# Performance work log

Hardware: AMD Instinct MI355X
Metric: run time of the kernel (lower is better)

## Reference

```python
import jax, jax.numpy as jnp
import numpy as np

# tf.image.rgb_to_grayscale luma weights; grayscale->rgb duplicates channels, so the
# rgb->gray after an identical per-channel gather reduces to scaling by sum(weights).
RGB_WSUM = np.float32(0.2989 + 0.5870 + 0.1140)


def _inverse_logpolar_indices(H, W):
    """Nearest-neighbor gather indices mapping a log-polar image (theta rows,
    rho cols) back to Cartesian coordinates (inverse log-polar remap)."""
    cy, cx = (H - 1) / 2.0, (W - 1) / 2.0
    ys, xs = np.meshgrid(np.arange(H, dtype=np.float64),
                         np.arange(W, dtype=np.float64), indexing='ij')
    dy, dx = ys - cy, xs - cx
    r = np.sqrt(dx * dx + dy * dy)
    rmax = np.sqrt(cx * cx + cy * cy)
    rho = np.where(r > 0.5, np.log(np.maximum(r, 1e-6)) / np.log(rmax) * (W - 1), 0.0)
    theta = (np.arctan2(dy, dx) + np.pi) / (2.0 * np.pi) * (H - 1)
    rho_i = np.clip(np.rint(rho), 0, W - 1).astype(np.int32)
    th_i = np.clip(np.rint(theta), 0, H - 1).astype(np.int32)
    return jnp.asarray(th_i), jnp.asarray(rho_i)  # each (H, W)


def setup_inputs() -> dict:
    key = jax.random.key(0)
    B, H, W, C = 1, 256, 256, 512
    inputs = jax.random.normal(key, (B, H, W, C), dtype=jnp.float32)
    return {"inputs": inputs}


def reference(inputs) -> jnp.ndarray:
    B, H, W, C = inputs.shape  # H == W required by the original layer's transpose/reshape
    # tf.transpose(tf.squeeze(inputs,0)) reverses all dims: (H,W,C) -> (C,W,H);
    # each channel is then tf.reshape'd to (H,W) (identity in memory for H==W).
    x = jnp.transpose(inputs[0], (2, 1, 0))  # (C, W, H) == (C, H, W) layout for square
    th_i, rho_i = _inverse_logpolar_indices(H, W)
    # Vectorized over channels: identical gather for every channel (replaces tf.map_fn).
    warped = x[:, th_i, rho_i]  # (C, H, W) irregular gather
    out = warped * RGB_WSUM      # gray->rgb (tile) -> warp -> rgb->gray collapses to a scale
    # tf.reshape((C,H,W) -> self.shape=(1,H,W,C)) is a raw row-major reshape (faithful).
    return jnp.reshape(out, (1, H, W, C))
```

## Files before the change

### kernel.cpp

```cpp
#include <hip/hip_runtime.h>
#include <math.h>


typedef float v4f __attribute__((ext_vector_type(4)));

__global__ __launch_bounds__(256) void InverseLogPolar_kernel(
        const float* __restrict__ in, float* __restrict__ out) {
    __shared__ int sBase[256];
    const int t    = threadIdx.x;
    const int pix0 = blockIdx.x << 8;
    const int c0   = blockIdx.y << 6;

    {
        const int g = pix0 + t;
        const int i = g >> 8;
        const int j = g & 255;
        const double dy = (double)i - 127.5;
        const double dx = (double)j - 127.5;
        const double r  = sqrt(dx * dx + dy * dy);
        const double rmax  = sqrt(127.5 * 127.5 + 127.5 * 127.5);
        const double lrmax = log(rmax);
        double rho   = (r > 0.5) ? (log(fmax(r, 1e-6)) / lrmax) * 255.0 : 0.0;
        double theta = ((atan2(dy, dx) + M_PI) / (2.0 * M_PI)) * 255.0;
        double rr = fmin(fmax(rint(rho),   0.0), 255.0);
        double tt = fmin(fmax(rint(theta), 0.0), 255.0);
        const int rho_i = (int)rr;
        const int th_i  = (int)tt;
        sBase[t] = (rho_i << 17) | (th_i << 9);
    }
    __syncthreads();

    const int l = t & 63;
    const int w = t >> 6;
    const int4 b4 = *reinterpret_cast<const int4*>(&sBase[l << 2]);
    const float WSUM = (float)(0.2989 + 0.587 + 0.114);
    const int pl = pix0 + (l << 2);

    #pragma unroll
    for (int itc = 0; itc < 4; ++itc) {
        const int c = c0 + (w << 4) + (itc << 2);
        const float4 v0 = *reinterpret_cast<const float4*>(in + b4.x + c);
        const float4 v1 = *reinterpret_cast<const float4*>(in + b4.y + c);
        const float4 v2 = *reinterpret_cast<const float4*>(in + b4.z + c);
        const float4 v3 = *reinterpret_cast<const float4*>(in + b4.w + c);

        v4f o0 = { v0.x * WSUM, v1.x * WSUM, v2.x * WSUM, v3.x * WSUM };
        v4f o1 = { v0.y * WSUM, v1.y * WSUM, v2.y * WSUM, v3.y * WSUM };
        v4f o2 = { v0.z * WSUM, v1.z * WSUM, v2.z * WSUM, v3.z * WSUM };
        v4f o3 = { v0.w * WSUM, v1.w * WSUM, v2.w * WSUM, v3.w * WSUM };

        __builtin_nontemporal_store(o0, reinterpret_cast<v4f*>(out + ((size_t)(c + 0) << 16) + pl));
        __builtin_nontemporal_store(o1, reinterpret_cast<v4f*>(out + ((size_t)(c + 1) << 16) + pl));
        __builtin_nontemporal_store(o2, reinterpret_cast<v4f*>(out + ((size_t)(c + 2) << 16) + pl));
        __builtin_nontemporal_store(o3, reinterpret_cast<v4f*>(out + ((size_t)(c + 3) << 16) + pl));
    }
}

extern "C" void kernel_launch(void* const* d_in, const int* in_sizes, int n_in,
                              void* d_out, int out_size, void* d_ws, size_t ws_size,
                              hipStream_t stream) {
    const float* in = (const float*)d_in[0];
    float* out = (float*)d_out;
    dim3 grid(256, 8);
    dim3 block(256);
    hipLaunchKernelGGL(InverseLogPolar_kernel, grid, block, 0, stream, in, out);
}
```

Before: 40.26 us.

## Transpose gathered channels through shared memory for coalesced gather loads

Each block now gathers 32 channels per pixel, with 8 threads sharing a pixel so every pixel's 128-byte channel run is read contiguously. The values are staged in a padded shared-memory tile and read back in channel-major order for the output stores. The channel block is halved and the grid doubled. This targets the scattered 16-byte reads of the previous layout, where each thread touched four different pixels, at the cost of 33 KB of LDS per block, an extra barrier, and more blocks that each recompute the double-precision index math.

Result: faster. 37.48 us (-6.9%).

```diff
diff --git a/kernel.cpp b/kernel.cpp
--- a/kernel.cpp
+++ b/kernel.cpp
@@ -6,10 +6,12 @@
 
 __global__ __launch_bounds__(256) void InverseLogPolar_kernel(
         const float* __restrict__ in, float* __restrict__ out) {
-    __shared__ int sBase[256];
+    __shared__ int   sBase[256];
+    __shared__ float tile[32 * 260];
+
     const int t    = threadIdx.x;
     const int pix0 = blockIdx.x << 8;
-    const int c0   = blockIdx.y << 6;
+    const int c0   = blockIdx.y << 5;
 
     {
         const int g = pix0 + t;
@@ -24,35 +26,40 @@
         double theta = ((atan2(dy, dx) + M_PI) / (2.0 * M_PI)) * 255.0;
         double rr = fmin(fmax(rint(rho),   0.0), 255.0);
         double tt = fmin(fmax(rint(theta), 0.0), 255.0);
-        const int rho_i = (int)rr;
-        const int th_i  = (int)tt;
-        sBase[t] = (rho_i << 17) | (th_i << 9);
+        sBase[t] = ((int)rr << 17) | ((int)tt << 9);
+    }
+    __syncthreads();
+
+    const float WSUM = (float)(0.2989 + 0.587 + 0.114);
+
+    float4 v[8];
+    #pragma unroll
+    for (int it = 0; it < 8; ++it) {
+        const int k = (it << 8) + t;
+        const int p = k >> 3;
+        const int cj = (k & 7) << 2;
+        v[it] = *reinterpret_cast<const float4*>(in + sBase[p] + c0 + cj);
+    }
+    #pragma unroll
+    for (int it = 0; it < 8; ++it) {
+        const int k = (it << 8) + t;
+        const int p = k >> 3;
+        const int cj = (k & 7) << 2;
+        tile[(cj + 0) * 260 + p] = v[it].x * WSUM;
+        tile[(cj + 1) * 260 + p] = v[it].y * WSUM;
+        tile[(cj + 2) * 260 + p] = v[it].z * WSUM;
+        tile[(cj + 3) * 260 + p] = v[it].w * WSUM;
     }
     __syncthreads();
 
     const int l = t & 63;
     const int w = t >> 6;
-    const int4 b4 = *reinterpret_cast<const int4*>(&sBase[l << 2]);
-    const float WSUM = (float)(0.2989 + 0.587 + 0.114);
-    const int pl = pix0 + (l << 2);
-
     #pragma unroll
-    for (int itc = 0; itc < 4; ++itc) {
-        const int c = c0 + (w << 4) + (itc << 2);
-        const float4 v0 = *reinterpret_cast<const float4*>(in + b4.x + c);
-        const float4 v1 = *reinterpret_cast<const float4*>(in + b4.y + c);
-        const float4 v2 = *reinterpret_cast<const float4*>(in + b4.z + c);
-        const float4 v3 = *reinterpret_cast<const float4*>(in + b4.w + c);
-
-        v4f o0 = { v0.x * WSUM, v1.x * WSUM, v2.x * WSUM, v3.x * WSUM };
-        v4f o1 = { v0.y * WSUM, v1.y * WSUM, v2.y * WSUM, v3.y * WSUM };
-        v4f o2 = { v0.z * WSUM, v1.z * WSUM, v2.z * WSUM, v3.z * WSUM };
-        v4f o3 = { v0.w * WSUM, v1.w * WSUM, v2.w * WSUM, v3.w * WSUM };
-
-        __builtin_nontemporal_store(o0, reinterpret_cast<v4f*>(out + ((size_t)(c + 0) << 16) + pl));
-        __builtin_nontemporal_store(o1, reinterpret_cast<v4f*>(out + ((size_t)(c + 1) << 16) + pl));
-        __builtin_nontemporal_store(o2, reinterpret_cast<v4f*>(out + ((size_t)(c + 2) << 16) + pl));
-        __builtin_nontemporal_store(o3, reinterpret_cast<v4f*>(out + ((size_t)(c + 3) << 16) + pl));
+    for (int it2 = 0; it2 < 8; ++it2) {
+        const int c = (w << 3) + it2;
+        const v4f o = *reinterpret_cast<const v4f*>(&tile[c * 260 + (l << 2)]);
+        __builtin_nontemporal_store(
+            o, reinterpret_cast<v4f*>(out + ((size_t)(c0 + c) << 16) + pix0 + (l << 2)));
     }
 }
 
@@ -61,7 +68,7 @@
                               hipStream_t stream) {
     const float* in = (const float*)d_in[0];
     float* out = (float*)d_out;
-    dim3 grid(256, 8);
+    dim3 grid(256, 16);
     dim3 block(256);
     hipLaunchKernelGGL(InverseLogPolar_kernel, grid, block, 0, stream, in, out);
 }
```
